# Kernel tuning notes

Hardware: AMD Instinct MI355X
Metric: run time of the kernel (lower is better)

Reference implementation:

```python
import jax, jax.numpy as jnp
import numpy as np

T, B, F, H = 8192, 1, 1024, 2048


def setup_inputs() -> dict:
    key = jax.random.key(0)
    ks = jax.random.split(key, 7)
    s = 1.0 / np.sqrt(H).astype(np.float32)  # PyTorch LSTM init scale
    u = lambda k, shape: jax.random.uniform(k, shape, jnp.float32, -s, s)
    return {
        "input": jax.random.normal(ks[0], (T, B, F), jnp.float32),
        "W_ih": u(ks[1], (4 * H, F)),
        "W_hh": u(ks[2], (4 * H, H)),
        "b_ih": u(ks[3], (4 * H,)),
        "b_hh": u(ks[4], (4 * H,)),
        "W_out": u(ks[5], (1, H)),
        "b_out": u(ks[6], (1,)),
    }


def reference(input, W_ih, W_hh, b_ih, b_hh, W_out, b_out):
    # input: [T, B, F] (seq-major, PyTorch default). h0 = c0 = 0.
    Tn, Bn, _ = input.shape
    Hn = W_hh.shape[1]
    # Precompute input contribution to all gates for every timestep: [T, B, 4H]
    x_gates = jnp.einsum('tbf,gf->tbg', input, W_ih) + b_ih + b_hh

    def step(carry, xg_t):
        h, c = carry                       # [B, H] each
        gates = xg_t + h @ W_hh.T          # [B, 4H]; PyTorch order i, f, g, o
        i, f, g, o = jnp.split(gates, 4, axis=-1)
        c_new = jax.nn.sigmoid(f) * c + jax.nn.sigmoid(i) * jnp.tanh(g)
        h_new = jax.nn.sigmoid(o) * jnp.tanh(c_new)
        return (h_new, c_new), h_new

    h0 = jnp.zeros((Bn, Hn), input.dtype)
    c0 = jnp.zeros((Bn, Hn), input.dtype)
    _, lstm_out = jax.lax.scan(step, (h0, c0), x_gates)  # [T, B, H]
    return lstm_out @ W_out.T + b_out                    # [T, B, 1]
```

## Files before the change

kernel.cpp:

```cpp
#include <hip/hip_runtime.h>
#include <hip/hip_bf16.h>

typedef unsigned short u16;
typedef unsigned int u32;
typedef unsigned long long u64;
typedef __fp16 f16x2 __attribute__((ext_vector_type(2)));
typedef int i32x4 __attribute__((ext_vector_type(4)));

#define T_  8192
#define F_  1024
#define H_  2048
#define G_  8192

#define NREG  8
#define DSLOT 4

#define WS_XG    0
#define WS_ABF   134217728ull
#define WS_WBF   150994944ull
#define WS_HX    167772160ull
#define WS_PART  168296448ull

static __device__ __forceinline__ float bf2f(u16 u) {
    union { u32 i; float f; } x; x.i = ((u32)u) << 16; return x.f;
}
static __device__ __forceinline__ u16 f2bf(float f) {
    union { float f; u32 u; } x; x.f = f;
    u32 r = (x.u + 0x7fffu + ((x.u >> 16) & 1u)) >> 16;
    return (u16)r;
}

__global__ void cvt4_kernel(const float* __restrict__ s, u16* __restrict__ d, int n4) {
    int i = blockIdx.x * 256 + threadIdx.x;
    if (i < n4) {
        float4 v = ((const float4*)s)[i];
        union { u16 h[4]; uint2 v2; } o;
        o.h[0] = f2bf(v.x); o.h[1] = f2bf(v.y); o.h[2] = f2bf(v.z); o.h[3] = f2bf(v.w);
        ((uint2*)d)[i] = o.v2;
    }
}

__global__ __launch_bounds__(256) void gemm_xg_kernel(
    const u16* __restrict__ A, const u16* __restrict__ W,
    const float* __restrict__ b_ih, const float* __restrict__ b_hh,
    u16* __restrict__ xg)
{
    __shared__ u16 As[64][40];
    __shared__ u16 Ws[64][40];

    const int tb = blockIdx.y * 64;
    const int gb = blockIdx.x * 64;
    const int tid  = threadIdx.x;
    const int wave = tid >> 6;
    const int lane = tid & 63;
    const int m    = lane & 15;
    const int quad = lane >> 4;

    const int lrow = tid >> 2;
    const int lcol = (tid & 3) * 8;

    using frag  = __attribute__((ext_vector_type(8))) short;
    using f32x4 = __attribute__((ext_vector_type(4))) float;
    f32x4 acc[4] = {};

    for (int k0 = 0; k0 < F_; k0 += 32) {
        __syncthreads();
        *(uint4*)&As[lrow][lcol] = *(const uint4*)&A[(size_t)(tb + lrow) * F_ + k0 + lcol];
        *(uint4*)&Ws[lrow][lcol] = *(const uint4*)&W[(size_t)(gb + lrow) * F_ + k0 + lcol];
        __syncthreads();
        frag bfr = *(const frag*)&Ws[wave * 16 + m][quad * 8];
#pragma unroll
        for (int i = 0; i < 4; ++i) {
            frag afr = *(const frag*)&As[i * 16 + m][quad * 8];
            acc[i] = __builtin_amdgcn_mfma_f32_16x16x32_bf16(afr, bfr, acc[i], 0, 0, 0);
        }
    }
    const int g = gb + wave * 16 + m;
    const float bias = b_ih[g] + b_hh[g];
#pragma unroll
    for (int i = 0; i < 4; ++i)
#pragma unroll
        for (int r = 0; r < 4; ++r) {
            int t = tb + i * 16 + quad * 4 + r;
            xg[(size_t)t * G_ + g] = f2bf(acc[i][r] + bias);
        }
}

__global__ __launch_bounds__(512, 2) void lstm_rec_kernel(
    const float* __restrict__ Whh,
    const u16*  __restrict__ xg,
    const float* __restrict__ Wout,
    u32*  __restrict__ hx,
    float* __restrict__ part)
{
    __shared__ u32 hs2[2][H_ / 2];
    __shared__ float pl[2][8];
    __shared__ u32 hpub[8];

    const int b   = blockIdx.x;
    const int tid = threadIdx.x;
    const int w   = tid >> 6;
    const int l   = tid & 63;
    const int uu  = b * 8 + w;

    f16x2 wreg[4][16];
#pragma unroll
    for (int r = 0; r < 4; ++r) {
        const float* wrow = Whh + (size_t)(r * H_ + uu) * H_;
#pragma unroll
        for (int kc = 0; kc < 16; ++kc) {
            float2 v = *(const float2*)&wrow[2 * (l + 64 * kc)];
            wreg[r][kc] = __builtin_amdgcn_cvt_pkrtz(v.x, v.y);
        }
    }
    const float wout = Wout[uu];
    float c = 0.f;

    hs2[1][tid] = 0; hs2[1][tid + 512] = 0;
    __syncthreads();

    float xgi, xgf, xgg, xgo;
    {
        const u16* xr = &xg[uu];
        xgi = bf2f(xr[0]); xgf = bf2f(xr[2048]);
        xgg = bf2f(xr[4096]); xgo = bf2f(xr[6144]);
    }

    const u32* mybase = hx + (size_t)(b & (NREG - 1)) * DSLOT * 2048;

    for (int t = 0; t < T_; ++t) {
        const u32* hsrc = hs2[(t & 1) ^ 1];

        if (tid == 17 && t > 0) {
            const float* q = pl[(t - 1) & 1];
            part[(size_t)(t - 1) * 256 + b] =
                q[0] + q[1] + q[2] + q[3] + q[4] + q[5] + q[6] + q[7];
        }

        float a0 = 0.f, a1 = 0.f, a2 = 0.f, a3 = 0.f;
#pragma unroll
        for (int kc = 0; kc < 16; ++kc) {
            union { u32 u; f16x2 h; } hw;
            hw.u = hsrc[l + 64 * kc];
            a0 = __builtin_amdgcn_fdot2(wreg[0][kc], hw.h, a0, false);
            a1 = __builtin_amdgcn_fdot2(wreg[1][kc], hw.h, a1, false);
            a2 = __builtin_amdgcn_fdot2(wreg[2][kc], hw.h, a2, false);
            a3 = __builtin_amdgcn_fdot2(wreg[3][kc], hw.h, a3, false);
        }
#pragma unroll
        for (int off = 32; off >= 1; off >>= 1) {
            a0 += __shfl_xor(a0, off);
            a1 += __shfl_xor(a1, off);
            a2 += __shfl_xor(a2, off);
            a3 += __shfl_xor(a3, off);
        }

        float gi = a0 + xgi, gf = a1 + xgf, gg = a2 + xgg, go = a3 + xgo;
        float i_ = 1.f / (1.f + __expf(-gi));
        float f_ = 1.f / (1.f + __expf(-gf));
        float g_ = 1.f - 2.f / (__expf(2.f * gg) + 1.f);
        float o_ = 1.f / (1.f + __expf(-go));
        c = fmaf(f_, c, i_ * g_);
        float th = 1.f - 2.f / (__expf(2.f * c) + 1.f);
        float hval = o_ * th;

        const int slot = t & (DSLOT - 1);

        u32 word;
        {
            union { __fp16 hh; u16 us; } cv; cv.hh = (__fp16)hval;
            word = ((u32)cv.us << 16) | (u32)(t & 0xffff);
        }
        if (l == 0) hpub[w] = word;
        if (l == 17) pl[t & 1][w] = hval * wout;
        __syncthreads();

        if (w == 0) {
            u32 v = hpub[l & 7];
            __hip_atomic_store(&hx[((size_t)(l >> 3) * DSLOT + slot) * 2048 + 8 * b + (l & 7)],
                               v, __ATOMIC_RELAXED, __HIP_MEMORY_SCOPE_AGENT);
        }

        float nxi = 0.f, nxf = 0.f, nxg = 0.f, nxo = 0.f;
        if (t + 1 < T_) {
            const u16* xr = &xg[(size_t)(t + 1) * G_ + uu];
            nxi = bf2f(xr[0]); nxf = bf2f(xr[2048]);
            nxg = bf2f(xr[4096]); nxo = bf2f(xr[6144]);
        }

        {
            const u32* pb = mybase + (size_t)slot * 2048 + 4 * tid;
            const u32 te = (u32)(t & 0xffff);
            i32x4 v;
            auto attempt = [&]() -> bool {
                asm volatile("global_load_dwordx4 %0, %1, off sc0 sc1\n\t"
                             "s_waitcnt vmcnt(0)"
                             : "=v"(v) : "v"(pb) : "memory");
                return (((u32)v.x & 0xffffu) == te) & (((u32)v.y & 0xffffu) == te) &
                       (((u32)v.z & 0xffffu) == te) & (((u32)v.w & 0xffffu) == te);
            };
            if (!attempt()) {
                __builtin_amdgcn_s_sleep(1);
                if (!attempt()) {
                    __builtin_amdgcn_s_sleep(2);
                    if (!attempt()) {
                        __builtin_amdgcn_s_sleep(4);
                        while (!attempt()) __builtin_amdgcn_s_sleep(8);
                    }
                }
            }
            u32* dst = hs2[t & 1];
            dst[2 * tid]     = (((u32)v.x) >> 16) | (((u32)v.y) & 0xffff0000u);
            dst[2 * tid + 1] = (((u32)v.z) >> 16) | (((u32)v.w) & 0xffff0000u);
        }
        xgi = nxi; xgf = nxf; xgg = nxg; xgo = nxo;
        __syncthreads();
    }

    if (tid == 17) {
        const float* q = pl[(T_ - 1) & 1];
        part[(size_t)(T_ - 1) * 256 + b] =
            q[0] + q[1] + q[2] + q[3] + q[4] + q[5] + q[6] + q[7];
    }
}

__global__ __launch_bounds__(256) void out_reduce_kernel(
    const float* __restrict__ part, const float* __restrict__ b_out,
    float* __restrict__ out)
{
    int t = blockIdx.x * 4 + (threadIdx.x >> 6);
    int l = threadIdx.x & 63;
    const float* p = &part[(size_t)t * 256];
    float s = p[l] + p[l + 64] + p[l + 128] + p[l + 192];
#pragma unroll
    for (int off = 32; off >= 1; off >>= 1) s += __shfl_down(s, off);
    if (l == 0) out[t] = s + b_out[0];
}

extern "C" void kernel_launch(void* const* d_in, const int* in_sizes, int n_in,
                              void* d_out, int out_size, void* d_ws, size_t ws_size,
                              hipStream_t stream) {
    const float* input = (const float*)d_in[0];
    const float* W_ih  = (const float*)d_in[1];
    const float* W_hh  = (const float*)d_in[2];
    const float* b_ih  = (const float*)d_in[3];
    const float* b_hh  = (const float*)d_in[4];
    const float* W_out = (const float*)d_in[5];
    const float* b_out = (const float*)d_in[6];
    float* out = (float*)d_out;

    char* ws = (char*)d_ws;
    u16*   xg   = (u16*)(ws + WS_XG);
    u16*   Abf  = (u16*)(ws + WS_ABF);
    u16*   Wbf  = (u16*)(ws + WS_WBF);
    u32*   hx   = (u32*)(ws + WS_HX);
    float* part = (float*)(ws + WS_PART);

    (void)hipMemsetAsync(hx, 0xFF, (size_t)NREG * DSLOT * 2048 * sizeof(u32), stream);

    const int n4 = (T_ * F_) / 4;
    cvt4_kernel<<<(n4 + 255) / 256, 256, 0, stream>>>(input, Abf, n4);
    cvt4_kernel<<<(G_ * F_ / 4 + 255) / 256, 256, 0, stream>>>(W_ih, Wbf, G_ * F_ / 4);

    gemm_xg_kernel<<<dim3(G_ / 64, T_ / 64), 256, 0, stream>>>(Abf, Wbf, b_ih, b_hh, xg);

    lstm_rec_kernel<<<256, 512, 0, stream>>>(W_hh, xg, W_out, hx, part);

    out_reduce_kernel<<<T_ / 4, 256, 0, stream>>>(part, b_out, out);
}
```

Baseline: 15.71 ms.

## Add helper wavefront to prefetch xg gates and write partial outputs

Adds a ninth wavefront to each recurrence block. It prefetches the xg gate inputs two steps ahead into a small shared ring buffer and writes the per-step output partial sums, so the eight compute wavefronts no longer issue those global loads or stores in the critical loop. This removes global memory latency from the compute waves' serial path. In exchange the block is larger (576 threads), the launch-bounds occupancy changes, and both __syncthreads calls per step now include the extra wave.

```diff
diff --git a/kernel.cpp b/kernel.cpp
--- a/kernel.cpp
+++ b/kernel.cpp
@@ -86,7 +86,7 @@
         }
 }
 
-__global__ __launch_bounds__(512, 2) void lstm_rec_kernel(
+__global__ __launch_bounds__(576, 2) void lstm_rec_kernel(
     const float* __restrict__ Whh,
     const u16*  __restrict__ xg,
     const float* __restrict__ Wout,
@@ -96,128 +96,137 @@
     __shared__ u32 hs2[2][H_ / 2];
     __shared__ float pl[2][8];
     __shared__ u32 hpub[8];
+    __shared__ u16 xgr[4][32];
 
     const int b   = blockIdx.x;
     const int tid = threadIdx.x;
     const int w   = tid >> 6;
     const int l   = tid & 63;
-    const int uu  = b * 8 + w;
+    const bool comp = (tid < 512);
+    const int uu  = b * 8 + (w & 7);
 
     f16x2 wreg[4][16];
-#pragma unroll
-    for (int r = 0; r < 4; ++r) {
-        const float* wrow = Whh + (size_t)(r * H_ + uu) * H_;
-#pragma unroll
-        for (int kc = 0; kc < 16; ++kc) {
-            float2 v = *(const float2*)&wrow[2 * (l + 64 * kc)];
-            wreg[r][kc] = __builtin_amdgcn_cvt_pkrtz(v.x, v.y);
-        }
-    }
-    const float wout = Wout[uu];
+    float wout = 0.f;
+    if (comp) {
+#pragma unroll
+        for (int r = 0; r < 4; ++r) {
+            const float* wrow = Whh + (size_t)(r * H_ + uu) * H_;
+#pragma unroll
+            for (int kc = 0; kc < 16; ++kc) {
+                float2 v = *(const float2*)&wrow[2 * (l + 64 * kc)];
+                wreg[r][kc] = __builtin_amdgcn_cvt_pkrtz(v.x, v.y);
+            }
+        }
+        wout = Wout[uu];
+    }
     float c = 0.f;
 
-    hs2[1][tid] = 0; hs2[1][tid + 512] = 0;
+    if (comp) { hs2[1][tid] = 0; hs2[1][tid + 512] = 0; }
+    else if (l < 32) {
+        const int r = l >> 3, u = l & 7;
+        xgr[0][l] = xg[(size_t)0 * G_ + r * H_ + b * 8 + u];
+        xgr[1][l] = xg[(size_t)1 * G_ + r * H_ + b * 8 + u];
+    }
     __syncthreads();
 
-    float xgi, xgf, xgg, xgo;
-    {
-        const u16* xr = &xg[uu];
-        xgi = bf2f(xr[0]); xgf = bf2f(xr[2048]);
-        xgg = bf2f(xr[4096]); xgo = bf2f(xr[6144]);
-    }
-
     const u32* mybase = hx + (size_t)(b & (NREG - 1)) * DSLOT * 2048;
 
     for (int t = 0; t < T_; ++t) {
-        const u32* hsrc = hs2[(t & 1) ^ 1];
-
-        if (tid == 17 && t > 0) {
-            const float* q = pl[(t - 1) & 1];
-            part[(size_t)(t - 1) * 256 + b] =
-                q[0] + q[1] + q[2] + q[3] + q[4] + q[5] + q[6] + q[7];
-        }
-
-        float a0 = 0.f, a1 = 0.f, a2 = 0.f, a3 = 0.f;
-#pragma unroll
-        for (int kc = 0; kc < 16; ++kc) {
-            union { u32 u; f16x2 h; } hw;
-            hw.u = hsrc[l + 64 * kc];
-            a0 = __builtin_amdgcn_fdot2(wreg[0][kc], hw.h, a0, false);
-            a1 = __builtin_amdgcn_fdot2(wreg[1][kc], hw.h, a1, false);
-            a2 = __builtin_amdgcn_fdot2(wreg[2][kc], hw.h, a2, false);
-            a3 = __builtin_amdgcn_fdot2(wreg[3][kc], hw.h, a3, false);
-        }
-#pragma unroll
-        for (int off = 32; off >= 1; off >>= 1) {
-            a0 += __shfl_xor(a0, off);
-            a1 += __shfl_xor(a1, off);
-            a2 += __shfl_xor(a2, off);
-            a3 += __shfl_xor(a3, off);
-        }
-
-        float gi = a0 + xgi, gf = a1 + xgf, gg = a2 + xgg, go = a3 + xgo;
-        float i_ = 1.f / (1.f + __expf(-gi));
-        float f_ = 1.f / (1.f + __expf(-gf));
-        float g_ = 1.f - 2.f / (__expf(2.f * gg) + 1.f);
-        float o_ = 1.f / (1.f + __expf(-go));
-        c = fmaf(f_, c, i_ * g_);
-        float th = 1.f - 2.f / (__expf(2.f * c) + 1.f);
-        float hval = o_ * th;
-
         const int slot = t & (DSLOT - 1);
-
-        u32 word;
-        {
-            union { __fp16 hh; u16 us; } cv; cv.hh = (__fp16)hval;
-            word = ((u32)cv.us << 16) | (u32)(t & 0xffff);
-        }
-        if (l == 0) hpub[w] = word;
-        if (l == 17) pl[t & 1][w] = hval * wout;
-        __syncthreads();
-
-        if (w == 0) {
-            u32 v = hpub[l & 7];
-            __hip_atomic_store(&hx[((size_t)(l >> 3) * DSLOT + slot) * 2048 + 8 * b + (l & 7)],
-                               v, __ATOMIC_RELAXED, __HIP_MEMORY_SCOPE_AGENT);
-        }
-
-        float nxi = 0.f, nxf = 0.f, nxg = 0.f, nxo = 0.f;
-        if (t + 1 < T_) {
-            const u16* xr = &xg[(size_t)(t + 1) * G_ + uu];
-            nxi = bf2f(xr[0]); nxf = bf2f(xr[2048]);
-            nxg = bf2f(xr[4096]); nxo = bf2f(xr[6144]);
-        }
-
-        {
-            const u32* pb = mybase + (size_t)slot * 2048 + 4 * tid;
-            const u32 te = (u32)(t & 0xffff);
-            i32x4 v;
-            auto attempt = [&]() -> bool {
-                asm volatile("global_load_dwordx4 %0, %1, off sc0 sc1\n\t"
-                             "s_waitcnt vmcnt(0)"
-                             : "=v"(v) : "v"(pb) : "memory");
-                return (((u32)v.x & 0xffffu) == te) & (((u32)v.y & 0xffffu) == te) &
-                       (((u32)v.z & 0xffffu) == te) & (((u32)v.w & 0xffffu) == te);
-            };
-            if (!attempt()) {
-                __builtin_amdgcn_s_sleep(1);
+        float hval = 0.f;
+
+        if (comp) {
+            const u32* hsrc = hs2[(t & 1) ^ 1];
+
+            const int s4 = t & 3;
+            u16 bxi = xgr[s4][w], bxf = xgr[s4][8 + w];
+            u16 bxg = xgr[s4][16 + w], bxo = xgr[s4][24 + w];
+
+            float a0 = 0.f, a1 = 0.f, a2 = 0.f, a3 = 0.f;
+#pragma unroll
+            for (int kc = 0; kc < 16; ++kc) {
+                union { u32 u; f16x2 h; } hw;
+                hw.u = hsrc[l + 64 * kc];
+                a0 = __builtin_amdgcn_fdot2(wreg[0][kc], hw.h, a0, false);
+                a1 = __builtin_amdgcn_fdot2(wreg[1][kc], hw.h, a1, false);
+                a2 = __builtin_amdgcn_fdot2(wreg[2][kc], hw.h, a2, false);
+                a3 = __builtin_amdgcn_fdot2(wreg[3][kc], hw.h, a3, false);
+            }
+#pragma unroll
+            for (int off = 32; off >= 1; off >>= 1) {
+                a0 += __shfl_xor(a0, off);
+                a1 += __shfl_xor(a1, off);
+                a2 += __shfl_xor(a2, off);
+                a3 += __shfl_xor(a3, off);
+            }
+
+            float gi = a0 + bf2f(bxi), gf = a1 + bf2f(bxf);
+            float gg = a2 + bf2f(bxg), go = a3 + bf2f(bxo);
+            float i_ = 1.f / (1.f + __expf(-gi));
+            float f_ = 1.f / (1.f + __expf(-gf));
+            float g_ = 1.f - 2.f / (__expf(2.f * gg) + 1.f);
+            float o_ = 1.f / (1.f + __expf(-go));
+            c = fmaf(f_, c, i_ * g_);
+            float th = 1.f - 2.f / (__expf(2.f * c) + 1.f);
+            hval = o_ * th;
+
+            u32 word;
+            {
+                union { __fp16 hh; u16 us; } cv; cv.hh = (__fp16)hval;
+                word = ((u32)cv.us << 16) | (u32)(t & 0xffff);
+            }
+            if (l == 0) hpub[w] = word;
+            if (l == 17) pl[t & 1][w] = hval * wout;
+        } else {
+            if (l == 32 && t > 0) {
+                const float* q = pl[(t - 1) & 1];
+                part[(size_t)(t - 1) * 256 + b] =
+                    q[0] + q[1] + q[2] + q[3] + q[4] + q[5] + q[6] + q[7];
+            }
+            if (l < 32 && t + 2 < T_) {
+                const int r = l >> 3, u = l & 7;
+                xgr[(t + 2) & 3][l] = xg[(size_t)(t + 2) * G_ + r * H_ + b * 8 + u];
+            }
+        }
+        __syncthreads();
+
+        if (comp) {
+            if (w == 0) {
+                u32 v = hpub[l & 7];
+                __hip_atomic_store(&hx[((size_t)(l >> 3) * DSLOT + slot) * 2048 + 8 * b + (l & 7)],
+                                   v, __ATOMIC_RELAXED, __HIP_MEMORY_SCOPE_AGENT);
+            }
+
+            {
+                const u32* pb = mybase + (size_t)slot * 2048 + 4 * tid;
+                const u32 te = (u32)(t & 0xffff);
+                i32x4 v;
+                auto attempt = [&]() -> bool {
+                    asm volatile("global_load_dwordx4 %0, %1, off sc0 sc1\n\t"
+                                 "s_waitcnt vmcnt(0)"
+                                 : "=v"(v) : "v"(pb) : "memory");
+                    return (((u32)v.x & 0xffffu) == te) & (((u32)v.y & 0xffffu) == te) &
+                           (((u32)v.z & 0xffffu) == te) & (((u32)v.w & 0xffffu) == te);
+                };
                 if (!attempt()) {
-                    __builtin_amdgcn_s_sleep(2);
+                    __builtin_amdgcn_s_sleep(1);
                     if (!attempt()) {
-                        __builtin_amdgcn_s_sleep(4);
-                        while (!attempt()) __builtin_amdgcn_s_sleep(8);
+                        __builtin_amdgcn_s_sleep(2);
+                        if (!attempt()) {
+                            __builtin_amdgcn_s_sleep(4);
+                            while (!attempt()) __builtin_amdgcn_s_sleep(8);
+                        }
                     }
                 }
-            }
-            u32* dst = hs2[t & 1];
-            dst[2 * tid]     = (((u32)v.x) >> 16) | (((u32)v.y) & 0xffff0000u);
-            dst[2 * tid + 1] = (((u32)v.z) >> 16) | (((u32)v.w) & 0xffff0000u);
-        }
-        xgi = nxi; xgf = nxf; xgg = nxg; xgo = nxo;
-        __syncthreads();
-    }
-
-    if (tid == 17) {
+                u32* dst = hs2[t & 1];
+                dst[2 * tid]     = (((u32)v.x) >> 16) | (((u32)v.y) & 0xffff0000u);
+                dst[2 * tid + 1] = (((u32)v.z) >> 16) | (((u32)v.w) & 0xffff0000u);
+            }
+        }
+        __syncthreads();
+    }
+
+    if (tid == 544) {
         const float* q = pl[(T_ - 1) & 1];
         part[(size_t)(T_ - 1) * 256 + b] =
             q[0] + q[1] + q[2] + q[3] + q[4] + q[5] + q[6] + q[7];
@@ -264,7 +273,7 @@
 
     gemm_xg_kernel<<<dim3(G_ / 64, T_ / 64), 256, 0, stream>>>(Abf, Wbf, b_ih, b_hh, xg);
 
-    lstm_rec_kernel<<<256, 512, 0, stream>>>(W_hh, xg, W_out, hx, part);
+    lstm_rec_kernel<<<256, 576, 0, stream>>>(W_hh, xg, W_out, hx, part);
 
     out_reduce_kernel<<<T_ / 4, 256, 0, stream>>>(part, b_out, out);
 }
```

New measurement: 23.18 ms. 47.5% more time.
